# Kernel tuning notes

Hardware: AMD Instinct MI355X
Metric: run time of the kernel (lower is better)

Reference implementation:

```python
import jax, jax.numpy as jnp
import numpy as np

N_NODES = 100000
N_EDGES = 1600000
IN_CH = 128
HID = 64
N_LAYERS = 4
OUT_CH = 10
NUM_GRAPHS = 128
BN_EPS = 1e-5


def setup_inputs() -> dict:
    key = jax.random.key(0)
    ks = jax.random.split(key, 24)
    s = 0.05
    inp = {
        "x": jax.random.normal(ks[0], (N_NODES, IN_CH), dtype=jnp.float32),
        "edge_index": jax.random.randint(ks[1], (2, N_EDGES), 0, N_NODES, dtype=jnp.int32),
        "batch": jnp.sort(jax.random.randint(ks[2], (N_NODES,), 0, NUM_GRAPHS, dtype=jnp.int32)),
        # GIN layer 0: MLP([IN_CH, HID, HID])
        "W1f": jax.random.normal(ks[3], (IN_CH, HID), dtype=jnp.float32) * s,
        "b1f": jnp.zeros((HID,), jnp.float32),
        "W2f": jax.random.normal(ks[4], (HID, HID), dtype=jnp.float32) * s,
        "b2f": jnp.zeros((HID,), jnp.float32),
        # GIN layers 1..3: MLP([HID, HID, HID]) each, stacked
        "W1r": jax.random.normal(ks[5], (N_LAYERS - 1, HID, HID), dtype=jnp.float32) * s,
        "b1r": jnp.zeros((N_LAYERS - 1, HID), jnp.float32),
        "W2r": jax.random.normal(ks[6], (N_LAYERS - 1, HID, HID), dtype=jnp.float32) * s,
        "b2r": jnp.zeros((N_LAYERS - 1, HID), jnp.float32),
        # JumpingKnowledge 'cat' projection: Linear(N_LAYERS*HID -> HID)
        "Wjk": jax.random.normal(ks[7], (N_LAYERS * HID, HID), dtype=jnp.float32) * s,
        "bjk": jnp.zeros((HID,), jnp.float32),
        # classifier MLP([HID, HID, OUT_CH]) with batch_norm
        "Wc1": jax.random.normal(ks[8], (HID, HID), dtype=jnp.float32) * s,
        "bc1": jnp.zeros((HID,), jnp.float32),
        "gamma": jnp.ones((HID,), jnp.float32),
        "beta": jnp.zeros((HID,), jnp.float32),
        "Wc2": jax.random.normal(ks[9], (HID, OUT_CH), dtype=jnp.float32) * s,
        "bc2": jnp.zeros((OUT_CH,), jnp.float32),
    }
    return inp


def _gin_conv(h, src, dst, W1, b1, W2, b2):
    # sum-aggregate messages from src to dst (eps = 0, so (1+eps)*x = x)
    agg = jax.ops.segment_sum(h[src], dst, num_segments=N_NODES)
    z = h + agg
    # GINConv nn: Linear -> ReLU -> Linear
    return jax.nn.relu(z @ W1 + b1) @ W2 + b2


def reference(x, edge_index, batch, W1f, b1f, W2f, b2f, W1r, b1r, W2r, b2r,
              Wjk, bjk, Wc1, bc1, gamma, beta, Wc2, bc2):
    src, dst = edge_index[0], edge_index[1]
    xs = []
    h = jax.nn.relu(_gin_conv(x, src, dst, W1f, b1f, W2f, b2f))  # post-conv act (dropout eval no-op)
    xs.append(h)
    for l in range(N_LAYERS - 1):
        h = jax.nn.relu(_gin_conv(h, src, dst, W1r[l], b1r[l], W2r[l], b2r[l]))
        xs.append(h)
    # JumpingKnowledge 'cat' + Linear
    h = jnp.concatenate(xs, axis=-1) @ Wjk + bjk            # [N, HID]
    # global add pool per graph
    pooled = jax.ops.segment_sum(h, batch, num_segments=NUM_GRAPHS)  # [G, HID]
    # classifier: Linear -> BatchNorm (batch stats) -> ReLU -> Linear
    z = pooled @ Wc1 + bc1
    mu = jnp.mean(z, axis=0)
    var = jnp.var(z, axis=0)
    z = gamma * (z - mu) * jax.lax.rsqrt(var + BN_EPS) + beta
    z = jax.nn.relu(z)
    return z @ Wc2 + bc2                                    # [G, OUT_CH]
```

## Files before the change

kernel.cpp:

```cpp
#include <hip/hip_runtime.h>
#include <hip/hip_bf16.h>

#define N_NODES    100000
#define N_EDGES    1600000
#define IN_CH      128
#define HID        64
#define N_LAYERS   4
#define OUT_CH     10
#define NUM_GRAPHS 128
#define BN_EPS     1e-5f
#define CAP        64
#define NREP       8
#define NBKT       256
#define NBUCK      196
#define EPB        2048
#define PNB        782
#define BCAP       10272

typedef __hip_bfloat16 bf16;
typedef unsigned int uint32;
typedef float f32x2 __attribute__((ext_vector_type(2)));
typedef float f32x4 __attribute__((ext_vector_type(4)));

__device__ __forceinline__ float bf2f(bf16 v) { return __bfloat162float(v); }
__device__ __forceinline__ f32x2 unpk2(uint32 p) {
    f32x2 r;
    r.x = __uint_as_float(p << 16);
    r.y = __uint_as_float(p & 0xffff0000u);
    return r;
}

__global__ void zero_i(int* __restrict__ p, int n) {
    int i = blockIdx.x * 256 + threadIdx.x;
    int st = gridDim.x * 256;
    for (; i < n; i += st) p[i] = 0;
}

__global__ void bhist(const int* __restrict__ dst, int* __restrict__ ghist) {
    __shared__ int h[NBKT];
    int t = threadIdx.x;
    h[t] = 0;
    __syncthreads();
    long base = (long)blockIdx.x * EPB;
    for (int u = 0; u < 8; u++) {
        long e = base + u * 256 + t;
        if (e < N_EDGES) atomicAdd(&h[dst[e] >> 9], 1);
    }
    __syncthreads();
    if (h[t]) atomicAdd(&ghist[t], h[t]);
}

__global__ void bscan(const int* __restrict__ ghist, int* __restrict__ gcursor,
                      int* __restrict__ gbase,
                      const int* __restrict__ batch, int* __restrict__ cntg,
                      bf16* __restrict__ ybfA, bf16* __restrict__ ybfB) {
    __shared__ int sh[NBKT];
    int t = threadIdx.x;
    int v = ghist[t];
    sh[t] = v;
    __syncthreads();
    for (int off = 1; off < NBKT; off <<= 1) {
        int a = (t >= off) ? sh[t - off] : 0;
        __syncthreads();
        sh[t] += a;
        __syncthreads();
    }
    gcursor[t] = sh[t] - v;
    gbase[t]   = sh[t] - v;
    if (t < NUM_GRAPHS) {
        int g = t, lo = 0, hi = N_NODES;
        while (lo < hi) { int m = (lo + hi) >> 1; if (batch[m] < g) lo = m + 1; else hi = m; }
        int lb = lo;
        lo = 0; hi = N_NODES;
        while (lo < hi) { int m = (lo + hi) >> 1; if (batch[m] < g + 1) lo = m + 1; else hi = m; }
        cntg[g] = lo - lb;
    }
    if (t < HID) {
        ybfA[(long)N_NODES * HID + t] = __float2bfloat16(0.f);
        ybfB[(long)N_NODES * HID + t] = __float2bfloat16(0.f);
    }
}

__global__ void bpart(const int* __restrict__ src, const int* __restrict__ dst,
                      int* __restrict__ gcursor, int* __restrict__ epart) {
    __shared__ int h[NBKT];
    __shared__ int cur[NBKT];
    int t = threadIdx.x;
    h[t] = 0;
    __syncthreads();
    long base = (long)blockIdx.x * EPB;
    int myd[8], mys[8];
    for (int u = 0; u < 8; u++) {
        long e = base + u * 256 + t;
        if (e < N_EDGES) {
            myd[u] = dst[e];
            mys[u] = src[e];
            atomicAdd(&h[myd[u] >> 9], 1);
        } else myd[u] = -1;
    }
    __syncthreads();
    if (h[t]) cur[t] = atomicAdd(&gcursor[t], h[t]);
    __syncthreads();
    for (int u = 0; u < 8; u++) {
        if (myd[u] >= 0) {
            int pos = atomicAdd(&cur[myd[u] >> 9], 1);
            epart[pos] = mys[u] | ((myd[u] & 511) << 17);
        }
    }
}

__global__ __launch_bounds__(256)
void bfill(const int* __restrict__ epart, const int* __restrict__ gbase,
           const int* __restrict__ ghist, int* __restrict__ cnt,
           int* __restrict__ col) {
    __shared__ int lcnt[512];
    __shared__ int loff[512];
    __shared__ int psum[256];
    __shared__ int lsrc[BCAP];
    const int b = blockIdx.x;
    const int t = threadIdx.x;
    const int n0 = b << 9;
    const int nN = min(512, N_NODES - n0);
    const int base = gbase[b];
    const int m = ghist[b];

    lcnt[t] = 0; lcnt[t + 256] = 0;
    __syncthreads();
    for (int e = t; e < m; e += 256)
        atomicAdd(&lcnt[(uint32)epart[base + e] >> 17], 1);
    __syncthreads();
    int c0 = lcnt[2 * t], c1 = lcnt[2 * t + 1];
    psum[t] = c0 + c1;
    __syncthreads();
    for (int off = 1; off < 256; off <<= 1) {
        int a = (t >= off) ? psum[t - off] : 0;
        __syncthreads();
        psum[t] += a;
        __syncthreads();
    }
    int eb = psum[t] - (c0 + c1);
    loff[2 * t] = eb;
    loff[2 * t + 1] = eb + c0;
    lcnt[2 * t] = 0; lcnt[2 * t + 1] = 0;
    __syncthreads();
    for (int e = t; e < m; e += 256) {
        uint32 v = (uint32)epart[base + e];
        int ln = v >> 17;
        int slot = atomicAdd(&lcnt[ln], 1);
        lsrc[loff[ln] + slot] = (int)(v & 0x1FFFFu);
    }
    __syncthreads();
    for (int ln = t; ln < nN; ln += 256) {
        int deg = lcnt[ln];
        int st  = loff[ln];
        int n   = n0 + ln;
        cnt[n] = deg;
        int d32 = (deg + 31) & ~31;
        int* row = col + n * CAP;
        for (int s4 = 0; s4 < d32; s4 += 4) {
            int4 q;
            q.x = (s4 + 0 < deg) ? lsrc[st + s4 + 0] : N_NODES;
            q.y = (s4 + 1 < deg) ? lsrc[st + s4 + 1] : N_NODES;
            q.z = (s4 + 2 < deg) ? lsrc[st + s4 + 2] : N_NODES;
            q.w = (s4 + 3 < deg) ? lsrc[st + s4 + 3] : N_NODES;
            *(int4*)(row + s4) = q;
        }
    }
}

__global__ void proj0(const float* __restrict__ x, const float* __restrict__ W1,
                      bf16* __restrict__ ybf) {
    __shared__ __align__(16) float xshT[4][IN_CH][4];
    const int wave = threadIdx.x >> 6, lane = threadIdx.x & 63;
    const int nb = blockIdx.x * 16 + wave * 4;
    #pragma unroll
    for (int r = 0; r < 4; r++) {
        float2 v = ((const float2*)(x + (long)(nb + r) * IN_CH))[lane];
        xshT[wave][2 * lane][r]     = v.x;
        xshT[wave][2 * lane + 1][r] = v.y;
    }
    f32x2 aA = {0.f, 0.f}, aB = {0.f, 0.f};
    #pragma unroll 8
    for (int k = 0; k < IN_CH; k++) {
        f32x4 q = *(const f32x4*)&xshT[wave][k][0];
        float w = W1[k * 64 + lane];
        f32x2 wv = {w, w};
        aA += (f32x2){q.x, q.y} * wv;
        aB += (f32x2){q.z, q.w} * wv;
    }
    ybf[(long)(nb + 0) * 64 + lane] = __float2bfloat16(aA.x);
    ybf[(long)(nb + 1) * 64 + lane] = __float2bfloat16(aA.y);
    ybf[(long)(nb + 2) * 64 + lane] = __float2bfloat16(aB.x);
    ybf[(long)(nb + 3) * 64 + lane] = __float2bfloat16(aB.y);
}

template <bool HAS_NEXT>
__global__ __launch_bounds__(256, 6)
void layer_fused(const bf16* __restrict__ ybf, const int* __restrict__ cnt,
                 const int* __restrict__ col, const int* __restrict__ batch,
                 const float* __restrict__ b1, const float* __restrict__ W2,
                 const float* __restrict__ b2, const float* __restrict__ W1n,
                 bf16* __restrict__ ynext, float* __restrict__ pooled_l) {
    __shared__ float csh[4][8][65];
    __shared__ float tsh[4][4][HID];
    __shared__ float hsh[4][4][HID];
    __shared__ float psh[4][HID];
    const int wave = threadIdx.x >> 6, lane = threadIdx.x & 63;
    const int eg = lane >> 3;
    const int j  = lane & 7;
    const uint32 joff = (uint32)j * 16u;
    const int nA = blockIdx.x * 16;
    const int nW = nA + wave * 4;
    const char* ybase = (const char*)ybf;

    #pragma unroll
    for (int r = 0; r < 4; r++) {
        const int n = __builtin_amdgcn_readfirstlane(nW + r);
        const int deg32 = __builtin_amdgcn_readfirstlane((cnt[n] + 31) & ~31);
        const int s = n * CAP;
        float acc[8] = {0.f, 0.f, 0.f, 0.f, 0.f, 0.f, 0.f, 0.f};
        for (int i = 0; i < deg32; i += 32) {
            uint4 p[4];
            #pragma unroll
            for (int t = 0; t < 4; t++) {
                int c = col[s + i + 8 * t + eg];
                uint32 off = ((uint32)c << 7) + joff;
                p[t] = *(const uint4*)(ybase + off);
            }
            #pragma unroll
            for (int t = 0; t < 4; t++) {
                f32x2 f0 = unpk2(p[t].x); acc[0] += f0.x; acc[1] += f0.y;
                f32x2 f1 = unpk2(p[t].y); acc[2] += f1.x; acc[3] += f1.y;
                f32x2 f2 = unpk2(p[t].z); acc[4] += f2.x; acc[5] += f2.y;
                f32x2 f3 = unpk2(p[t].w); acc[6] += f3.x; acc[7] += f3.y;
            }
        }
        #pragma unroll
        for (int d = 0; d < 8; d++) csh[wave][eg][8 * j + d] = acc[d];
        float sumv = 0.f;
        #pragma unroll
        for (int ee = 0; ee < 8; ee++) sumv += csh[wave][ee][lane];
        float t = bf2f(ybf[(long)n * 64 + lane]) + b1[lane] + sumv;
        tsh[wave][r][lane] = fmaxf(t, 0.f);
    }

    float hv0, hv1, hv2, hv3;
    {
        const float bb = b2[lane];
        float h0 = bb, h1 = bb, h2 = bb, h3 = bb;
        for (int k = 0; k < 64; k += 4) {
            float4 t0 = *(const float4*)&tsh[wave][0][k];
            float4 t1 = *(const float4*)&tsh[wave][1][k];
            float4 t2 = *(const float4*)&tsh[wave][2][k];
            float4 t3 = *(const float4*)&tsh[wave][3][k];
            float w0 = W2[(k + 0) * 64 + lane];
            float w1 = W2[(k + 1) * 64 + lane];
            float w2 = W2[(k + 2) * 64 + lane];
            float w3 = W2[(k + 3) * 64 + lane];
            h0 += t0.x * w0 + t0.y * w1 + t0.z * w2 + t0.w * w3;
            h1 += t1.x * w0 + t1.y * w1 + t1.z * w2 + t1.w * w3;
            h2 += t2.x * w0 + t2.y * w1 + t2.z * w2 + t2.w * w3;
            h3 += t3.x * w0 + t3.y * w1 + t3.z * w2 + t3.w * w3;
        }
        hv0 = fmaxf(h0, 0.f); hv1 = fmaxf(h1, 0.f);
        hv2 = fmaxf(h2, 0.f); hv3 = fmaxf(h3, 0.f);
    }
    hsh[wave][0][lane] = hv0;
    hsh[wave][1][lane] = hv1;
    hsh[wave][2][lane] = hv2;
    hsh[wave][3][lane] = hv3;

    if (HAS_NEXT) {
        float y0 = 0.f, y1 = 0.f, y2 = 0.f, y3 = 0.f;
        for (int k = 0; k < 64; k += 4) {
            float4 g0 = *(const float4*)&hsh[wave][0][k];
            float4 g1 = *(const float4*)&hsh[wave][1][k];
            float4 g2 = *(const float4*)&hsh[wave][2][k];
            float4 g3 = *(const float4*)&hsh[wave][3][k];
            float w0 = W1n[(k + 0) * 64 + lane];
            float w1 = W1n[(k + 1) * 64 + lane];
            float w2 = W1n[(k + 2) * 64 + lane];
            float w3 = W1n[(k + 3) * 64 + lane];
            y0 += g0.x * w0 + g0.y * w1 + g0.z * w2 + g0.w * w3;
            y1 += g1.x * w0 + g1.y * w1 + g1.z * w2 + g1.w * w3;
            y2 += g2.x * w0 + g2.y * w1 + g2.z * w2 + g2.w * w3;
            y3 += g3.x * w0 + g3.y * w1 + g3.z * w2 + g3.w * w3;
        }
        ynext[(long)(nW + 0) * 64 + lane] = __float2bfloat16(y0);
        ynext[(long)(nW + 1) * 64 + lane] = __float2bfloat16(y1);
        ynext[(long)(nW + 2) * 64 + lane] = __float2bfloat16(y2);
        ynext[(long)(nW + 3) * 64 + lane] = __float2bfloat16(y3);
    }

    const int gA = __builtin_amdgcn_readfirstlane(batch[nA]);
    const int gZ = __builtin_amdgcn_readfirstlane(batch[nA + 15]);
    float* rep = pooled_l + (long)(blockIdx.x & (NREP - 1)) * NUM_GRAPHS * HID;
    if (gA == gZ) {
        psh[wave][lane] = (hv0 + hv1) + (hv2 + hv3);
        __syncthreads();
        if (wave == 0) {
            float ssum = (psh[0][lane] + psh[1][lane]) + (psh[2][lane] + psh[3][lane]);
            atomicAdd(&rep[gA * 64 + lane], ssum);
        }
    } else {
        const int g0 = __builtin_amdgcn_readfirstlane(batch[nW + 0]);
        atomicAdd(&rep[g0 * 64 + lane], hv0);
        const int g1 = __builtin_amdgcn_readfirstlane(batch[nW + 1]);
        atomicAdd(&rep[g1 * 64 + lane], hv1);
        const int g2 = __builtin_amdgcn_readfirstlane(batch[nW + 2]);
        atomicAdd(&rep[g2 * 64 + lane], hv2);
        const int g3 = __builtin_amdgcn_readfirstlane(batch[nW + 3]);
        atomicAdd(&rep[g3 * 64 + lane], hv3);
    }
}

__global__ void jk_cls1(const float* __restrict__ pooled, const int* __restrict__ cntg,
                        const float* __restrict__ Wjk, const float* __restrict__ bjk,
                        const float* __restrict__ Wc1, const float* __restrict__ bc1,
                        float* __restrict__ Z, float* __restrict__ zstats) {
    __shared__ __align__(16) float sh[4][HID];
    __shared__ float pacc[4][HID];
    __shared__ __align__(16) float pj[HID];
    __shared__ float zacc[4][HID];
    const int g = blockIdx.x;
    const int wave = threadIdx.x >> 6, j = threadIdx.x & 63;

    float s = 0.f;
    for (int r = 0; r < NREP; r++)
        s += pooled[((long)(wave * NREP + r) * NUM_GRAPHS + g) * 64 + j];
    sh[wave][j] = s;
    const float* W = Wjk + (long)wave * HID * 64;
    float a = 0.f;
    for (int k = 0; k < 64; k += 4) {
        f32x4 sv = *(const f32x4*)&sh[wave][k];
        a += sv.x * W[(k + 0) * 64 + j];
        a += sv.y * W[(k + 1) * 64 + j];
        a += sv.z * W[(k + 2) * 64 + j];
        a += sv.w * W[(k + 3) * 64 + j];
    }
    pacc[wave][j] = a;
    __syncthreads();

    if (wave == 0)
        pj[j] = (float)cntg[g] * bjk[j]
              + (pacc[0][j] + pacc[1][j]) + (pacc[2][j] + pacc[3][j]);
    __syncthreads();

    float z = 0.f;
    for (int k = 16 * wave; k < 16 * wave + 16; k += 4) {
        f32x4 pv = *(const f32x4*)&pj[k];
        z += pv.x * Wc1[(k + 0) * 64 + j];
        z += pv.y * Wc1[(k + 1) * 64 + j];
        z += pv.z * Wc1[(k + 2) * 64 + j];
        z += pv.w * Wc1[(k + 3) * 64 + j];
    }
    zacc[wave][j] = z;
    __syncthreads();
    if (wave == 0) {
        float zv = bc1[j] + (zacc[0][j] + zacc[1][j]) + (zacc[2][j] + zacc[3][j]);
        Z[g * 64 + j] = zv;
        atomicAdd(&zstats[j], zv);
        atomicAdd(&zstats[HID + j], zv * zv);
    }
}

__global__ void cls2(const float* __restrict__ Z, const float* __restrict__ zstats,
                     const float* __restrict__ gamma, const float* __restrict__ beta,
                     const float* __restrict__ Wc2, const float* __restrict__ bc2,
                     float* __restrict__ out) {
    __shared__ float v[HID];
    const int g = blockIdx.x, j = threadIdx.x;
    float mu = zstats[j] * (1.f / NUM_GRAPHS);
    float var = zstats[HID + j] * (1.f / NUM_GRAPHS) - mu * mu;
    float rs = rsqrtf(var + BN_EPS);
    float zv = Z[g * 64 + j];
    v[j] = fmaxf(gamma[j] * (zv - mu) * rs + beta[j], 0.f);
    if (j < OUT_CH) {
        float acc = bc2[j];
        for (int k = 0; k < 64; k++) acc += v[k] * Wc2[k * OUT_CH + j];
        out[g * OUT_CH + j] = acc;
    }
}

extern "C" void kernel_launch(void* const* d_in, const int* in_sizes, int n_in,
                              void* d_out, int out_size, void* d_ws, size_t ws_size,
                              hipStream_t stream) {
    const float* x     = (const float*)d_in[0];
    const int*   ei    = (const int*)d_in[1];
    const int*   batch = (const int*)d_in[2];
    const float* W1f   = (const float*)d_in[3];
    const float* b1f   = (const float*)d_in[4];
    const float* W2f   = (const float*)d_in[5];
    const float* b2f   = (const float*)d_in[6];
    const float* W1r   = (const float*)d_in[7];
    const float* b1r   = (const float*)d_in[8];
    const float* W2r   = (const float*)d_in[9];
    const float* b2r   = (const float*)d_in[10];
    const float* Wjk   = (const float*)d_in[11];
    const float* bjk   = (const float*)d_in[12];
    const float* Wc1   = (const float*)d_in[13];
    const float* bc1   = (const float*)d_in[14];
    const float* gamma = (const float*)d_in[15];
    const float* beta  = (const float*)d_in[16];
    const float* Wc2   = (const float*)d_in[17];
    const float* bc2   = (const float*)d_in[18];

    const int* src = ei;
    const int* dst = ei + N_EDGES;

    float* ws        = (float*)d_ws;
    float* Z         = ws;
    bf16*  ybfA      = (bf16*)(Z + NUM_GRAPHS * HID);
    bf16*  ybfB      = ybfA + (long)(N_NODES + 1) * HID;
    int*   cnt       = (int*)(ybfB + (long)(N_NODES + 1) * HID);
    float* pooled    = (float*)(cnt + N_NODES);
    int*   ghist     = (int*)(pooled + (long)N_LAYERS * NREP * NUM_GRAPHS * HID);
    int*   gcursor   = ghist + NBKT;
    int*   gbase     = gcursor + NBKT;
    int*   cntg      = gbase + NBKT;
    float* zstats    = (float*)(cntg + NUM_GRAPHS);
    int*   col       = (int*)(zstats + 2 * HID);
    int*   epart     = col + (long)N_NODES * CAP;
    const int ZN = N_LAYERS * NREP * NUM_GRAPHS * HID
                 + 3 * NBKT + NUM_GRAPHS + 2 * HID;

    zero_i<<<360, 256, 0, stream>>>((int*)pooled, ZN);
    bhist<<<PNB, 256, 0, stream>>>(dst, ghist);
    bscan<<<1, 256, 0, stream>>>(ghist, gcursor, gbase, batch, cntg, ybfA, ybfB);
    bpart<<<PNB, 256, 0, stream>>>(src, dst, gcursor, epart);
    bfill<<<NBUCK, 256, 0, stream>>>(epart, gbase, ghist, cnt, col);

    proj0<<<N_NODES / 16, 256, 0, stream>>>(x, W1f, ybfA);

    const int NB = N_NODES / 16;
    const long PL = (long)NREP * NUM_GRAPHS * HID;
    layer_fused<true><<<NB, 256, 0, stream>>>(
        ybfA, cnt, col, batch, b1f, W2f, b2f,
        W1r, ybfB, pooled);
    layer_fused<true><<<NB, 256, 0, stream>>>(
        ybfB, cnt, col, batch, b1r, W2r, b2r,
        W1r + (long)1 * HID * HID, ybfA, pooled + 1 * PL);
    layer_fused<true><<<NB, 256, 0, stream>>>(
        ybfA, cnt, col, batch, b1r + HID, W2r + (long)1 * HID * HID, b2r + HID,
        W1r + (long)2 * HID * HID, ybfB, pooled + 2 * PL);
    layer_fused<false><<<NB, 256, 0, stream>>>(
        ybfB, cnt, col, batch, b1r + 2 * HID, W2r + (long)2 * HID * HID, b2r + 2 * HID,
        nullptr, nullptr, pooled + 3 * PL);

    jk_cls1<<<NUM_GRAPHS, 256, 0, stream>>>(pooled, cntg, Wjk, bjk, Wc1, bc1,
                                            Z, zstats);
    cls2<<<NUM_GRAPHS, 64, 0, stream>>>(Z, zstats, gamma, beta, Wc2, bc2,
                                        (float*)d_out);
}
```

Baseline: 427.8 us.

## Merge histogram, zeroing and input projection into one launch; split bfill per bucket

The edge-bucket histogram, the workspace zeroing and the layer-0 input projection now run as one kernel, with block index ranges selecting the role, so they overlap and two launches go away. ghist is moved out of the zeroed region and cleared by a tiny separate kernel before the histogram runs. bfill now uses four blocks per 512-node bucket, each covering 128 nodes with a smaller LDS buffer. That raises parallelism and occupancy, but each block rescans the whole bucket's edge list, so epart reads are quadrupled.

```diff
diff --git a/kernel.cpp b/kernel.cpp
--- a/kernel.cpp
+++ b/kernel.cpp
@@ -15,7 +15,9 @@
 #define NBUCK      196
 #define EPB        2048
 #define PNB        782
-#define BCAP       10272
+#define SUBCAP     2688
+#define ZB         360
+#define P0B        6250
 
 typedef __hip_bfloat16 bf16;
 typedef unsigned int uint32;
@@ -36,18 +38,51 @@
     for (; i < n; i += st) p[i] = 0;
 }
 
-__global__ void bhist(const int* __restrict__ dst, int* __restrict__ ghist) {
-    __shared__ int h[NBKT];
-    int t = threadIdx.x;
-    h[t] = 0;
-    __syncthreads();
-    long base = (long)blockIdx.x * EPB;
-    for (int u = 0; u < 8; u++) {
-        long e = base + u * 256 + t;
-        if (e < N_EDGES) atomicAdd(&h[dst[e] >> 9], 1);
-    }
-    __syncthreads();
-    if (h[t]) atomicAdd(&ghist[t], h[t]);
+__global__ void stage1(const int* __restrict__ dst, int* __restrict__ ghist,
+                       int* __restrict__ zp, int zn,
+                       const float* __restrict__ x, const float* __restrict__ W1,
+                       bf16* __restrict__ ybf) {
+    const int bid = blockIdx.x;
+    const int t = threadIdx.x;
+    if (bid < PNB) {
+        __shared__ int h[NBKT];
+        h[t] = 0;
+        __syncthreads();
+        long base = (long)bid * EPB;
+        for (int u = 0; u < 8; u++) {
+            long e = base + u * 256 + t;
+            if (e < N_EDGES) atomicAdd(&h[dst[e] >> 9], 1);
+        }
+        __syncthreads();
+        if (h[t]) atomicAdd(&ghist[t], h[t]);
+    } else if (bid < PNB + ZB) {
+        int i = (bid - PNB) * 256 + t;
+        const int st = ZB * 256;
+        for (; i < zn; i += st) zp[i] = 0;
+    } else {
+        __shared__ __align__(16) float xshT[4][IN_CH][4];
+        const int wave = t >> 6, lane = t & 63;
+        const int nb = (bid - PNB - ZB) * 16 + wave * 4;
+        #pragma unroll
+        for (int r = 0; r < 4; r++) {
+            float2 v = ((const float2*)(x + (long)(nb + r) * IN_CH))[lane];
+            xshT[wave][2 * lane][r]     = v.x;
+            xshT[wave][2 * lane + 1][r] = v.y;
+        }
+        f32x2 aA = {0.f, 0.f}, aB = {0.f, 0.f};
+        #pragma unroll 8
+        for (int k = 0; k < IN_CH; k++) {
+            f32x4 q = *(const f32x4*)&xshT[wave][k][0];
+            float w = W1[k * 64 + lane];
+            f32x2 wv = {w, w};
+            aA += (f32x2){q.x, q.y} * wv;
+            aB += (f32x2){q.z, q.w} * wv;
+        }
+        ybf[(long)(nb + 0) * 64 + lane] = __float2bfloat16(aA.x);
+        ybf[(long)(nb + 1) * 64 + lane] = __float2bfloat16(aA.y);
+        ybf[(long)(nb + 2) * 64 + lane] = __float2bfloat16(aB.x);
+        ybf[(long)(nb + 3) * 64 + lane] = __float2bfloat16(aB.y);
+    }
 }
 
 __global__ void bscan(const int* __restrict__ ghist, int* __restrict__ gcursor,
@@ -113,85 +148,64 @@
 void bfill(const int* __restrict__ epart, const int* __restrict__ gbase,
            const int* __restrict__ ghist, int* __restrict__ cnt,
            int* __restrict__ col) {
-    __shared__ int lcnt[512];
-    __shared__ int loff[512];
-    __shared__ int psum[256];
-    __shared__ int lsrc[BCAP];
-    const int b = blockIdx.x;
+    __shared__ int lcnt[128];
+    __shared__ int loff[128];
+    __shared__ int lsrc[SUBCAP];
+    const int b = blockIdx.x >> 2;
+    const int q = blockIdx.x & 3;
     const int t = threadIdx.x;
-    const int n0 = b << 9;
-    const int nN = min(512, N_NODES - n0);
+    const int n0 = (b << 9) + (q << 7);
+    if (n0 >= N_NODES) return;
+    const int nN = min(128, N_NODES - n0);
     const int base = gbase[b];
     const int m = ghist[b];
-
-    lcnt[t] = 0; lcnt[t + 256] = 0;
-    __syncthreads();
-    for (int e = t; e < m; e += 256)
-        atomicAdd(&lcnt[(uint32)epart[base + e] >> 17], 1);
-    __syncthreads();
-    int c0 = lcnt[2 * t], c1 = lcnt[2 * t + 1];
-    psum[t] = c0 + c1;
-    __syncthreads();
-    for (int off = 1; off < 256; off <<= 1) {
-        int a = (t >= off) ? psum[t - off] : 0;
-        __syncthreads();
-        psum[t] += a;
-        __syncthreads();
-    }
-    int eb = psum[t] - (c0 + c1);
-    loff[2 * t] = eb;
-    loff[2 * t + 1] = eb + c0;
-    lcnt[2 * t] = 0; lcnt[2 * t + 1] = 0;
+    const int lo = q << 7;
+
+    if (t < 128) lcnt[t] = 0;
+    __syncthreads();
+    for (int e = t; e < m; e += 256) {
+        int ln = (int)((uint32)epart[base + e] >> 17) - lo;
+        if ((uint32)ln < 128u) atomicAdd(&lcnt[ln], 1);
+    }
+    __syncthreads();
+    if (t < 128) loff[t] = lcnt[t];
+    __syncthreads();
+    for (int off = 1; off < 128; off <<= 1) {
+        int a = (t < 128 && t >= off) ? loff[t - off] : 0;
+        __syncthreads();
+        if (t < 128) loff[t] += a;
+        __syncthreads();
+    }
+    int ex = 0;
+    if (t < 128) ex = loff[t] - lcnt[t];
+    __syncthreads();
+    if (t < 128) { loff[t] = ex; lcnt[t] = 0; }
     __syncthreads();
     for (int e = t; e < m; e += 256) {
         uint32 v = (uint32)epart[base + e];
-        int ln = v >> 17;
-        int slot = atomicAdd(&lcnt[ln], 1);
-        lsrc[loff[ln] + slot] = (int)(v & 0x1FFFFu);
-    }
-    __syncthreads();
-    for (int ln = t; ln < nN; ln += 256) {
-        int deg = lcnt[ln];
-        int st  = loff[ln];
-        int n   = n0 + ln;
+        int ln = (int)(v >> 17) - lo;
+        if ((uint32)ln < 128u) {
+            int slot = atomicAdd(&lcnt[ln], 1);
+            lsrc[loff[ln] + slot] = (int)(v & 0x1FFFFu);
+        }
+    }
+    __syncthreads();
+    if (t < nN) {
+        int deg = lcnt[t];
+        int st  = loff[t];
+        int n   = n0 + t;
         cnt[n] = deg;
         int d32 = (deg + 31) & ~31;
         int* row = col + n * CAP;
         for (int s4 = 0; s4 < d32; s4 += 4) {
-            int4 q;
-            q.x = (s4 + 0 < deg) ? lsrc[st + s4 + 0] : N_NODES;
-            q.y = (s4 + 1 < deg) ? lsrc[st + s4 + 1] : N_NODES;
-            q.z = (s4 + 2 < deg) ? lsrc[st + s4 + 2] : N_NODES;
-            q.w = (s4 + 3 < deg) ? lsrc[st + s4 + 3] : N_NODES;
-            *(int4*)(row + s4) = q;
-        }
-    }
-}
-
-__global__ void proj0(const float* __restrict__ x, const float* __restrict__ W1,
-                      bf16* __restrict__ ybf) {
-    __shared__ __align__(16) float xshT[4][IN_CH][4];
-    const int wave = threadIdx.x >> 6, lane = threadIdx.x & 63;
-    const int nb = blockIdx.x * 16 + wave * 4;
-    #pragma unroll
-    for (int r = 0; r < 4; r++) {
-        float2 v = ((const float2*)(x + (long)(nb + r) * IN_CH))[lane];
-        xshT[wave][2 * lane][r]     = v.x;
-        xshT[wave][2 * lane + 1][r] = v.y;
-    }
-    f32x2 aA = {0.f, 0.f}, aB = {0.f, 0.f};
-    #pragma unroll 8
-    for (int k = 0; k < IN_CH; k++) {
-        f32x4 q = *(const f32x4*)&xshT[wave][k][0];
-        float w = W1[k * 64 + lane];
-        f32x2 wv = {w, w};
-        aA += (f32x2){q.x, q.y} * wv;
-        aB += (f32x2){q.z, q.w} * wv;
-    }
-    ybf[(long)(nb + 0) * 64 + lane] = __float2bfloat16(aA.x);
-    ybf[(long)(nb + 1) * 64 + lane] = __float2bfloat16(aA.y);
-    ybf[(long)(nb + 2) * 64 + lane] = __float2bfloat16(aB.x);
-    ybf[(long)(nb + 3) * 64 + lane] = __float2bfloat16(aB.y);
+            int4 qv;
+            qv.x = (s4 + 0 < deg) ? lsrc[st + s4 + 0] : N_NODES;
+            qv.y = (s4 + 1 < deg) ? lsrc[st + s4 + 1] : N_NODES;
+            qv.z = (s4 + 2 < deg) ? lsrc[st + s4 + 2] : N_NODES;
+            qv.w = (s4 + 3 < deg) ? lsrc[st + s4 + 3] : N_NODES;
+            *(int4*)(row + s4) = qv;
+        }
+    }
 }
 
 template <bool HAS_NEXT>
@@ -414,23 +428,23 @@
     bf16*  ybfB      = ybfA + (long)(N_NODES + 1) * HID;
     int*   cnt       = (int*)(ybfB + (long)(N_NODES + 1) * HID);
     float* pooled    = (float*)(cnt + N_NODES);
-    int*   ghist     = (int*)(pooled + (long)N_LAYERS * NREP * NUM_GRAPHS * HID);
-    int*   gcursor   = ghist + NBKT;
+    int*   gcursor   = (int*)(pooled + (long)N_LAYERS * NREP * NUM_GRAPHS * HID);
     int*   gbase     = gcursor + NBKT;
     int*   cntg      = gbase + NBKT;
     float* zstats    = (float*)(cntg + NUM_GRAPHS);
-    int*   col       = (int*)(zstats + 2 * HID);
+    int*   ghist     = (int*)(zstats + 2 * HID);
+    int*   col       = ghist + NBKT;
     int*   epart     = col + (long)N_NODES * CAP;
     const int ZN = N_LAYERS * NREP * NUM_GRAPHS * HID
-                 + 3 * NBKT + NUM_GRAPHS + 2 * HID;
-
-    zero_i<<<360, 256, 0, stream>>>((int*)pooled, ZN);
-    bhist<<<PNB, 256, 0, stream>>>(dst, ghist);
+                 + 2 * NBKT + NUM_GRAPHS + 2 * HID;
+
+    zero_i<<<1, 256, 0, stream>>>(ghist, NBKT);
+
+    stage1<<<PNB + ZB + P0B, 256, 0, stream>>>(dst, ghist, (int*)pooled, ZN,
+                                               x, W1f, ybfA);
     bscan<<<1, 256, 0, stream>>>(ghist, gcursor, gbase, batch, cntg, ybfA, ybfB);
     bpart<<<PNB, 256, 0, stream>>>(src, dst, gcursor, epart);
-    bfill<<<NBUCK, 256, 0, stream>>>(epart, gbase, ghist, cnt, col);
-
-    proj0<<<N_NODES / 16, 256, 0, stream>>>(x, W1f, ybfA);
+    bfill<<<NBUCK * 4, 256, 0, stream>>>(epart, gbase, ghist, cnt, col);
 
     const int NB = N_NODES / 16;
     const long PL = (long)NREP * NUM_GRAPHS * HID;
```

After: 422.7 us. About the same (-1.2%).
